# Optimization experiments

Hardware: AMD Instinct MI355X
Metric: run time of the kernel (lower is better)

Reference implementation:

```python
import jax, jax.numpy as jnp
import numpy as np


def setup_inputs() -> dict:
    key = jax.random.key(0)
    k1, k2 = jax.random.split(key)
    x = jax.random.normal(k1, (32, 128, 56, 56), dtype=jnp.float32)
    weight = jax.random.normal(k2, (256, 128, 3, 3), dtype=jnp.float32) * 0.01
    bias = jnp.zeros((256,), dtype=jnp.float32)
    return {"x": x, "weight": weight, "bias": bias}


def reference(x, weight, bias):
    # Faithful to Conv2dGEMM: im2col + GEMM is mathematically a standard
    # cross-correlation conv with the given stride/padding. We express it as
    # the efficient fused form (implicit GEMM) which computes identical math.
    stride, padding = 1, 1
    out = jax.lax.conv_general_dilated(
        x, weight,
        window_strides=(stride, stride),
        padding=[(padding, padding), (padding, padding)],
        dimension_numbers=("NCHW", "OIHW", "NCHW"),
    )  # [B, out_ch, H_out, W_out]
    return out + bias[None, :, None, None]
```

## Files before the change

### kernel.cpp

```cpp
#include <hip/hip_runtime.h>
#include <stdint.h>

typedef __bf16 bf16x8 __attribute__((ext_vector_type(8)));
typedef float  f32x4  __attribute__((ext_vector_type(4)));

#define NB   32
#define CI   128
#define HH   56
#define WW   56
#define CO   256
#define HP   58
#define HW   (HH*WW)
#define MTOT (NB*HW)
#define KTOT 1152

#define XT_ELEMS ((size_t)NB*HP*HP*CI)
#define XT_BYTES (XT_ELEMS*2)

__global__ void halo_zero(__bf16* __restrict__ xt) {
  int id = blockIdx.x * 256 + threadIdx.x;
  if (id >= NB * 228 * 16) return;
  int chunk = id & 15;
  int p = (id >> 4) % 228;
  int n = id / (228 * 16);
  int h, w;
  if (p < 58)       { h = 0;           w = p; }
  else if (p < 116) { h = 57;          w = p - 58; }
  else if (p < 172) { h = p - 116 + 1; w = 0; }
  else              { h = p - 172 + 1; w = 57; }
  int4* dst = (int4*)(xt + ((size_t)(n * HP + h) * HP + w) * CI) + chunk;
  *dst = make_int4(0, 0, 0, 0);
}

__global__ void xpose_kernel(const float* __restrict__ x, __bf16* __restrict__ xt) {
  int nh = blockIdx.x;
  int n = nh / HH, h = nh % HH;
  __shared__ float tile[CI][57];
  const float* src = x + (size_t)n * CI * HW + (size_t)h * WW;
  int t = threadIdx.x;
  for (int idx = t; idx < CI * 14; idx += 256) {
    int c = idx / 14, w4 = idx - c * 14;
    float4 v = *(const float4*)(src + (size_t)c * HW + w4 * 4);
    tile[c][w4 * 4 + 0] = v.x;
    tile[c][w4 * 4 + 1] = v.y;
    tile[c][w4 * 4 + 2] = v.z;
    tile[c][w4 * 4 + 3] = v.w;
  }
  __syncthreads();
  __bf16* dst = xt + ((size_t)(n * HP + h + 1) * HP + 1) * CI;
  for (int idx = t; idx < WW * 16; idx += 256) {
    int w = idx >> 4, c8 = (idx & 15) * 8;
    bf16x8 v;
    for (int k = 0; k < 8; ++k) v[k] = (__bf16)tile[c8 + k][w];
    *(bf16x8*)(dst + (size_t)w * CI + c8) = v;
  }
}

__global__ void wxform_kernel(const float* __restrict__ wg, __bf16* __restrict__ wt) {
  int id = blockIdx.x * 256 + threadIdx.x;
  int o = id / KTOT;
  int k = id - o * KTOT;
  int rs = k >> 7, c = k & 127;
  wt[id] = (__bf16)wg[(size_t)o * KTOT + c * 9 + rs];
}

#define BM 128
#define BN 128

__device__ __forceinline__ void gload_lds16(const __bf16* g, __bf16* l) {
  __builtin_amdgcn_global_load_lds(
      (const __attribute__((address_space(1))) void*)g,
      (__attribute__((address_space(3))) void*)l, 16, 0, 0);
}

__global__ __launch_bounds__(256, 3) void conv_gemm(
    const __bf16* __restrict__ xt, const __bf16* __restrict__ wt,
    const float* __restrict__ bias, float* __restrict__ out) {
  __shared__ __bf16 Alds[2][BM * 32];
  __shared__ __bf16 Blds[2][BN * 32];
  int t = threadIdx.x;
  int bx = blockIdx.x;
  int nb = bx & 1, mb = bx >> 1;

  size_t baseA[2], baseB[2];
  __bf16* ldsA[2][2];
  __bf16* ldsB[2][2];
  for (int i = 0; i < 2; ++i) {
    int ml = i * 64 + (t >> 2);
    unsigned m = mb * BM + ml;
    unsigned nimg = m / HW;
    unsigned hw = m - nimg * HW;
    unsigned h = hw / WW;
    unsigned w = hw - h * WW;
    baseA[i] = ((size_t)(nimg * HP + h) * HP + w) * CI + (t & 3) * 8;
    baseB[i] = (size_t)(nb * BN + ml) * KTOT + (t & 3) * 8;
    for (int p = 0; p < 2; ++p) {
      ldsA[i][p] = &Alds[p][ml * 32 + (t & 3) * 8];
      ldsB[i][p] = &Blds[p][ml * 32 + (t & 3) * 8];
    }
  }

  int wid = t >> 6, lane = t & 63;
  int wm = (wid >> 1) * 64, wn = (wid & 1) * 64;
  int lr = lane & 15, lk = (lane >> 4) * 8;

  f32x4 acc[4][4];
  for (int i = 0; i < 4; ++i)
    for (int j = 0; j < 4; ++j) acc[i][j] = (f32x4){0.f, 0.f, 0.f, 0.f};

  for (int kt = 0; kt < KTOT / 64; ++kt) {
    int rs = kt >> 1;
    int r = (rs * 11) >> 5;
    int s = rs - 3 * r;
    size_t offA = ((size_t)(r * HP + s)) * CI + (size_t)(kt & 1) * 64;
    size_t offB = (size_t)kt * 64;
    for (int p = 0; p < 2; ++p) {
      gload_lds16(xt + baseA[0] + offA + p * 32, ldsA[0][p]);
      gload_lds16(xt + baseA[1] + offA + p * 32, ldsA[1][p]);
      gload_lds16(wt + baseB[0] + offB + p * 32, ldsB[0][p]);
      gload_lds16(wt + baseB[1] + offB + p * 32, ldsB[1][p]);
    }
    __syncthreads();
    for (int p = 0; p < 2; ++p) {
      bf16x8 a[4], b[4];
      for (int i = 0; i < 4; ++i) {
        a[i] = *(const bf16x8*)&Alds[p][(wm + i * 16 + lr) * 32 + lk];
        b[i] = *(const bf16x8*)&Blds[p][(wn + i * 16 + lr) * 32 + lk];
      }
      for (int i = 0; i < 4; ++i)
        for (int j = 0; j < 4; ++j)
          acc[i][j] = __builtin_amdgcn_mfma_f32_16x16x32_bf16(a[i], b[j], acc[i][j], 0, 0, 0);
    }
    __syncthreads();
  }

  for (int j = 0; j < 4; ++j) {
    int o = nb * BN + wn + j * 16 + lr;
    float bv = bias[o];
    for (int i = 0; i < 4; ++i) {
      unsigned m0 = mb * BM + wm + i * 16 + (lane >> 4) * 4;
      for (int r2 = 0; r2 < 4; ++r2) {
        unsigned m = m0 + r2;
        unsigned nimg = m / HW;
        unsigned hw = m - nimg * HW;
        out[((size_t)nimg * CO + o) * HW + hw] = acc[i][j][r2] + bv;
      }
    }
  }
}

extern "C" void kernel_launch(void* const* d_in, const int* in_sizes, int n_in,
                              void* d_out, int out_size, void* d_ws, size_t ws_size,
                              hipStream_t stream) {
  const float* x    = (const float*)d_in[0];
  const float* wg   = (const float*)d_in[1];
  const float* bias = (const float*)d_in[2];
  float* out = (float*)d_out;

  __bf16* xt = (__bf16*)d_ws;
  __bf16* wt = (__bf16*)((char*)d_ws + XT_BYTES);

  halo_zero<<<(NB * 228 * 16 + 255) / 256, 256, 0, stream>>>(xt);
  xpose_kernel<<<NB * HH, 256, 0, stream>>>(x, xt);
  wxform_kernel<<<(CO * KTOT) / 256, 256, 0, stream>>>(wg, wt);
  conv_gemm<<<(MTOT / BM) * (CO / BN), 256, 0, stream>>>(xt, wt, bias, out);
}
```

Before: 224.3 us.

## Restructure conv GEMM into 128x256 tile with triple-buffered swizzled LDS pipeline

The GEMM block grows to 128x256 with 512 threads and K steps of 64 (18 iterations). Global-to-LDS loads go into a three-stage ring with XOR-swizzled layout, issued two steps ahead and interleaved with MFMA groups under s_setprio, gated by explicit vmcnt waits and one barrier per step. The epilogue also switches to vectorized float4 stores. This targets load latency, LDS bank conflicts and the double barrier per step, at the cost of 144KB of LDS and lower occupancy.

```diff
diff --git a/kernel.cpp b/kernel.cpp
--- a/kernel.cpp
+++ b/kernel.cpp
@@ -65,86 +65,136 @@
 }
 
 #define BM 128
-#define BN 128
-
-__device__ __forceinline__ void gload_lds16(const __bf16* g, __bf16* l) {
-  __builtin_amdgcn_global_load_lds(
-      (const __attribute__((address_space(1))) void*)g,
-      (__attribute__((address_space(3))) void*)l, 16, 0, 0);
-}
-
-__global__ __launch_bounds__(256, 3) void conv_gemm(
+#define BN 256
+#define NKT 18
+
+#define STAGE_A2(BS, OFF) \
+  { _Pragma("unroll") for (int i_ = 0; i_ < 2; ++i_) \
+      __builtin_amdgcn_global_load_lds( \
+        (const __attribute__((address_space(1))) void*)(xtc + baseA[i_] + (OFF)), \
+        (__attribute__((address_space(3))) void*)(lds + (BS)*16384 + i_*8192 + ldst), 16, 0, 0); }
+
+#define STAGE_B01(BS, OFF) \
+  { _Pragma("unroll") for (int i_ = 0; i_ < 2; ++i_) \
+      __builtin_amdgcn_global_load_lds( \
+        (const __attribute__((address_space(1))) void*)(wtc + baseB[i_] + (OFF)), \
+        (__attribute__((address_space(3))) void*)(lds + 49152 + (BS)*32768 + i_*8192 + ldst), 16, 0, 0); }
+
+#define STAGE_B23(BS, OFF) \
+  { _Pragma("unroll") for (int i_ = 2; i_ < 4; ++i_) \
+      __builtin_amdgcn_global_load_lds( \
+        (const __attribute__((address_space(1))) void*)(wtc + baseB[i_] + (OFF)), \
+        (__attribute__((address_space(3))) void*)(lds + 49152 + (BS)*32768 + i_*8192 + ldst), 16, 0, 0); }
+
+#define KBODY(KT, BC, BS, DOSTAGE, DOBAR, VMCLIT) do { \
+  int kt2_ = (KT) + 2; \
+  int rs2_ = kt2_ >> 1; int r2_ = (rs2_*11)>>5; int s2_ = rs2_ - 3*r2_; \
+  uint32_t offA2_ = (uint32_t)((r2_*HP + s2_) * 256 + (kt2_ & 1) * 128); \
+  uint32_t offB2_ = (uint32_t)(kt2_ * 128); \
+  const char* Ab_ = lds + (BC)*16384; \
+  const char* Bb_ = lds + 49152 + (BC)*32768; \
+  bf16x8 av_[4][2], bva_[2][2], bvb_[2][2]; \
+  _Pragma("unroll") for (int a_ = 0; a_ < 4; ++a_) { \
+    av_[a_][0] = *(const bf16x8*)(Ab_ + rowA + a_*2048 + slot0); \
+    av_[a_][1] = *(const bf16x8*)(Ab_ + rowA + a_*2048 + slot1); } \
+  _Pragma("unroll") for (int b_ = 0; b_ < 2; ++b_) { \
+    bva_[b_][0] = *(const bf16x8*)(Bb_ + rowB + b_*2048 + slot0); \
+    bva_[b_][1] = *(const bf16x8*)(Bb_ + rowB + b_*2048 + slot1); } \
+  if (DOSTAGE) { STAGE_A2(BS, offA2_); STAGE_B01(BS, offB2_); } \
+  __builtin_amdgcn_s_setprio(1); \
+  _Pragma("unroll") for (int a_ = 0; a_ < 4; ++a_) { \
+    _Pragma("unroll") for (int b_ = 0; b_ < 2; ++b_) { \
+      acc[a_][b_] = __builtin_amdgcn_mfma_f32_16x16x32_bf16(av_[a_][0], bva_[b_][0], acc[a_][b_], 0, 0, 0); \
+      acc[a_][b_] = __builtin_amdgcn_mfma_f32_16x16x32_bf16(av_[a_][1], bva_[b_][1], acc[a_][b_], 0, 0, 0); } } \
+  __builtin_amdgcn_s_setprio(0); \
+  _Pragma("unroll") for (int b_ = 0; b_ < 2; ++b_) { \
+    bvb_[b_][0] = *(const bf16x8*)(Bb_ + rowB + 4096 + b_*2048 + slot0); \
+    bvb_[b_][1] = *(const bf16x8*)(Bb_ + rowB + 4096 + b_*2048 + slot1); } \
+  if (DOSTAGE) { STAGE_B23(BS, offB2_); } \
+  __builtin_amdgcn_s_setprio(1); \
+  _Pragma("unroll") for (int a_ = 0; a_ < 4; ++a_) { \
+    _Pragma("unroll") for (int b_ = 0; b_ < 2; ++b_) { \
+      acc[a_][b_+2] = __builtin_amdgcn_mfma_f32_16x16x32_bf16(av_[a_][0], bvb_[b_][0], acc[a_][b_+2], 0, 0, 0); \
+      acc[a_][b_+2] = __builtin_amdgcn_mfma_f32_16x16x32_bf16(av_[a_][1], bvb_[b_][1], acc[a_][b_+2], 0, 0, 0); } } \
+  __builtin_amdgcn_s_setprio(0); \
+  if (DOBAR) { \
+    asm volatile("s_waitcnt vmcnt(" VMCLIT ")" ::: "memory"); \
+    __builtin_amdgcn_sched_barrier(0); \
+    __builtin_amdgcn_s_barrier(); \
+    __builtin_amdgcn_sched_barrier(0); } \
+} while (0)
+
+__global__ __launch_bounds__(512, 2) void conv_gemm(
     const __bf16* __restrict__ xt, const __bf16* __restrict__ wt,
     const float* __restrict__ bias, float* __restrict__ out) {
-  __shared__ __bf16 Alds[2][BM * 32];
-  __shared__ __bf16 Blds[2][BN * 32];
+  __shared__ char lds[147456];
   int t = threadIdx.x;
-  int bx = blockIdx.x;
-  int nb = bx & 1, mb = bx >> 1;
-
-  size_t baseA[2], baseB[2];
-  __bf16* ldsA[2][2];
-  __bf16* ldsB[2][2];
+  int mb = blockIdx.x;
+  const char* xtc = (const char*)xt;
+  const char* wtc = (const char*)wt;
+
+  int arow = t >> 3;
+  int kbsrc = ((t & 7) * 16) ^ ((arow & 7) << 4);
+  int ldst = t * 16;
+  uint32_t baseA[2];
+#pragma unroll
   for (int i = 0; i < 2; ++i) {
-    int ml = i * 64 + (t >> 2);
-    unsigned m = mb * BM + ml;
+    unsigned m = mb * BM + i * 64 + arow;
     unsigned nimg = m / HW;
     unsigned hw = m - nimg * HW;
     unsigned h = hw / WW;
     unsigned w = hw - h * WW;
-    baseA[i] = ((size_t)(nimg * HP + h) * HP + w) * CI + (t & 3) * 8;
-    baseB[i] = (size_t)(nb * BN + ml) * KTOT + (t & 3) * 8;
-    for (int p = 0; p < 2; ++p) {
-      ldsA[i][p] = &Alds[p][ml * 32 + (t & 3) * 8];
-      ldsB[i][p] = &Blds[p][ml * 32 + (t & 3) * 8];
-    }
-  }
+    baseA[i] = ((nimg * HP + h) * HP + w) * (CI * 2) + kbsrc;
+  }
+  uint32_t baseB[4];
+#pragma unroll
+  for (int i = 0; i < 4; ++i)
+    baseB[i] = (i * 64 + arow) * (KTOT * 2) + kbsrc;
 
   int wid = t >> 6, lane = t & 63;
-  int wm = (wid >> 1) * 64, wn = (wid & 1) * 64;
-  int lr = lane & 15, lk = (lane >> 4) * 8;
+  int wm = (wid >> 2) * 64;
+  int wn = (wid & 3) * 64;
+  int lr = lane & 15, hi = lane >> 4;
+  int swz = (lr & 7) << 4;
+  int slot0 = (hi * 16) ^ swz;
+  int slot1 = (64 + hi * 16) ^ swz;
+  int rowA = (wm + lr) * 128;
+  int rowB = (wn + lr) * 128;
 
   f32x4 acc[4][4];
+#pragma unroll
   for (int i = 0; i < 4; ++i)
+#pragma unroll
     for (int j = 0; j < 4; ++j) acc[i][j] = (f32x4){0.f, 0.f, 0.f, 0.f};
 
-  for (int kt = 0; kt < KTOT / 64; ++kt) {
-    int rs = kt >> 1;
-    int r = (rs * 11) >> 5;
-    int s = rs - 3 * r;
-    size_t offA = ((size_t)(r * HP + s)) * CI + (size_t)(kt & 1) * 64;
-    size_t offB = (size_t)kt * 64;
-    for (int p = 0; p < 2; ++p) {
-      gload_lds16(xt + baseA[0] + offA + p * 32, ldsA[0][p]);
-      gload_lds16(xt + baseA[1] + offA + p * 32, ldsA[1][p]);
-      gload_lds16(wt + baseB[0] + offB + p * 32, ldsB[0][p]);
-      gload_lds16(wt + baseB[1] + offB + p * 32, ldsB[1][p]);
-    }
-    __syncthreads();
-    for (int p = 0; p < 2; ++p) {
-      bf16x8 a[4], b[4];
-      for (int i = 0; i < 4; ++i) {
-        a[i] = *(const bf16x8*)&Alds[p][(wm + i * 16 + lr) * 32 + lk];
-        b[i] = *(const bf16x8*)&Blds[p][(wn + i * 16 + lr) * 32 + lk];
-      }
-      for (int i = 0; i < 4; ++i)
-        for (int j = 0; j < 4; ++j)
-          acc[i][j] = __builtin_amdgcn_mfma_f32_16x16x32_bf16(a[i], b[j], acc[i][j], 0, 0, 0);
-    }
-    __syncthreads();
-  }
-
+  STAGE_A2(0, 0u);   STAGE_B01(0, 0u);   STAGE_B23(0, 0u);
+  STAGE_A2(1, 128u); STAGE_B01(1, 128u); STAGE_B23(1, 128u);
+  asm volatile("s_waitcnt vmcnt(6)" ::: "memory");
+  __builtin_amdgcn_sched_barrier(0);
+  __builtin_amdgcn_s_barrier();
+  __builtin_amdgcn_sched_barrier(0);
+
+  for (int kt = 0; kt < 15; kt += 3) {
+    KBODY(kt + 0, 0, 2, 1, 1, "6");
+    KBODY(kt + 1, 1, 0, 1, 1, "6");
+    KBODY(kt + 2, 2, 1, 1, 1, "6");
+  }
+  KBODY(15, 0, 2, 1, 1, "6");
+  KBODY(16, 1, 0, 0, 1, "0");
+  KBODY(17, 2, 1, 0, 0, "0");
+
+#pragma unroll
   for (int j = 0; j < 4; ++j) {
-    int o = nb * BN + wn + j * 16 + lr;
+    int o = wn + j * 16 + lr;
     float bv = bias[o];
+#pragma unroll
     for (int i = 0; i < 4; ++i) {
-      unsigned m0 = mb * BM + wm + i * 16 + (lane >> 4) * 4;
-      for (int r2 = 0; r2 < 4; ++r2) {
-        unsigned m = m0 + r2;
-        unsigned nimg = m / HW;
-        unsigned hw = m - nimg * HW;
-        out[((size_t)nimg * CO + o) * HW + hw] = acc[i][j][r2] + bv;
-      }
+      unsigned m0 = mb * BM + wm + i * 16 + hi * 4;
+      unsigned nimg = m0 / HW;
+      unsigned hw = m0 - nimg * HW;
+      f32x4 v = acc[i][j];
+      v[0] += bv; v[1] += bv; v[2] += bv; v[3] += bv;
+      *(f32x4*)(out + ((size_t)nimg * CO + o) * HW + hw) = v;
     }
   }
 }
@@ -163,5 +213,5 @@
   halo_zero<<<(NB * 228 * 16 + 255) / 256, 256, 0, stream>>>(xt);
   xpose_kernel<<<NB * HH, 256, 0, stream>>>(x, xt);
   wxform_kernel<<<(CO * KTOT) / 256, 256, 0, stream>>>(wg, wt);
-  conv_gemm<<<(MTOT / BM) * (CO / BN), 256, 0, stream>>>(xt, wt, bias, out);
-}
+  conv_gemm<<<MTOT / BM, 512, 0, stream>>>(xt, wt, bias, out);
+}
```

New measurement: 218.5 us. -2.6%, faster.
